# Performance work log

Hardware: AMD Instinct MI355X
Metric: run time of the kernel (lower is better)

Reference implementation:

```python
import jax, jax.numpy as jnp
import numpy as np
from jax import lax

KS = 3            # kernel_size
K = 32            # cluster_num
NB = 32           # num_base_kernels
HID = 64          # mlp_hidden_dim
COUT = 64         # out_channels
MAX_ITER = 20
TOL = 0.005


def _unfold3(x):
    # torch nn.Unfold(k=3, pad=1): output channel order is (c, kh, kw)
    b, c, h, w = x.shape
    xp = jnp.pad(x, ((0, 0), (0, 0), (1, 1), (1, 1)))
    cols = [xp[:, :, i:i + h, j:j + w] for i in range(KS) for j in range(KS)]
    p = jnp.stack(cols, axis=2)  # [B, C, 9, H, W]
    return p.reshape(b, c * KS * KS, h * w).transpose(0, 2, 1)  # [B, HW, C*9]


def _kmeans_single(key, sample):
    # sample: [N, D]. Lloyd iterations with early stop on total center shift.
    n, d = sample.shape
    centers0 = sample[jax.random.permutation(key, n)[:K]]

    def assign(centers):
        d2 = (jnp.sum(sample * sample, 1, keepdims=True)
              - 2.0 * (sample @ centers.T)
              + jnp.sum(centers * centers, 1))
        return jnp.argmin(d2, axis=1)

    def body(carry):
        i, centers, _ = carry
        a = assign(centers)
        oh = jax.nn.one_hot(a, K, dtype=sample.dtype)  # [N, K]
        counts = oh.sum(0)                             # [K]
        sums = oh.T @ sample                           # [K, D]
        new = jnp.where(counts[:, None] > 0,
                        sums / jnp.maximum(counts, 1.0)[:, None],
                        centers)
        shift = jnp.sum(jnp.linalg.norm(new - centers, axis=1))
        return (i + 1, new, shift)

    def cond(carry):
        i, _, shift = carry
        return jnp.logical_and(i < MAX_ITER, shift >= TOL * n)

    init = (jnp.int32(0), centers0, jnp.asarray(jnp.inf, sample.dtype))
    _, centers, _ = lax.while_loop(cond, body, init)
    return assign(centers)


def _kmeans(features):
    keys = jax.random.split(jax.random.key(42), features.shape[0])
    return jax.vmap(_kmeans_single)(keys, features)


def _mlp(x, w1, b1, w2, b2, w3, b3):
    h = jax.nn.relu(x @ w1 + b1)
    h = jax.nn.relu(h @ w2 + b2)
    return h @ w3 + b3


def setup_inputs() -> dict:
    key = jax.random.key(0)
    ks = jax.random.split(key, 16)
    B, C, H, W = 2, 32, 64, 64
    F = C * KS * KS
    fan = 1.0 / np.sqrt(F)
    fanh = 1.0 / np.sqrt(HID)
    return {
        'x': jax.random.normal(ks[0], (B, C, H, W), jnp.float32),
        'base_kernels': jax.random.normal(ks[1], (NB, F, COUT), jnp.float32) * np.sqrt(2.0 / F),
        'kg_w1': jax.random.normal(ks[2], (F, HID), jnp.float32) * fan,
        'kg_b1': jnp.zeros((HID,), jnp.float32),
        'kg_w2': jax.random.normal(ks[3], (HID, HID), jnp.float32) * fanh,
        'kg_b2': jnp.zeros((HID,), jnp.float32),
        'kg_w3': jax.random.normal(ks[4], (HID, NB), jnp.float32) * fanh,
        'kg_b3': jnp.zeros((NB,), jnp.float32),
        'bg_w1': jax.random.normal(ks[5], (F, HID), jnp.float32) * fan,
        'bg_b1': jnp.zeros((HID,), jnp.float32),
        'bg_w2': jax.random.normal(ks[6], (HID, HID), jnp.float32) * fanh,
        'bg_b2': jnp.zeros((HID,), jnp.float32),
        'bg_w3': jax.random.normal(ks[7], (HID, COUT), jnp.float32) * fanh,
        'bg_b3': jnp.zeros((COUT,), jnp.float32),
    }


def reference(x, base_kernels, kg_w1, kg_b1, kg_w2, kg_b2, kg_w3, kg_b3,
              bg_w1, bg_b1, bg_w2, bg_b2, bg_w3, bg_b3):
    B, C, H, W = x.shape
    patches = _unfold3(x)  # [B, P, F] with F = C*9
    P = patches.shape[1]
    # observation features: mean over kernel area per channel
    obs = patches.reshape(B, P, C, KS * KS).mean(-1)  # [B, P, C]
    idx = _kmeans(obs)  # [B, P] int cluster assignments

    # per-cluster centers of the full patch features (scatter-mean)
    oh = jax.nn.one_hot(idx, K, dtype=patches.dtype)          # [B, P, K]
    sums = jnp.einsum('bpk,bpf->bkf', oh, patches)            # [B, K, F]
    counts = jnp.maximum(oh.sum(1), 1.0)                      # [B, K]
    centers = sums / counts[:, :, None]                       # [B, K, F]

    # adaptive kernels = softmax-mixture of base kernels
    attn = jax.nn.softmax(_mlp(centers, kg_w1, kg_b1, kg_w2, kg_b2, kg_w3, kg_b3), axis=-1)  # [B,K,NB]
    kernels = jnp.einsum('bkn,nfc->bkfc', attn, base_kernels)  # [B, K, F, COUT]
    biases = _mlp(centers, bg_w1, bg_b1, bg_w2, bg_b2, bg_w3, bg_b3)  # [B, K, COUT]

    # combine: out[b,p] = patches[b,p] @ kernels[b, idx[b,p]] + biases[b, idx[b,p]]
    bidx = jnp.arange(B)[:, None]
    wtok = kernels[bidx, idx]   # [B, P, F, COUT]
    btok = biases[bidx, idx]    # [B, P, COUT]
    out = jnp.einsum('bpf,bpfc->bpc', patches, wtok) + btok
    out = out.transpose(0, 2, 1).reshape(B, COUT, H, W)
    return (out, idx)
```

## Files before the change

kernel.cpp:

```cpp
#include <hip/hip_runtime.h>
#include <hip/hip_bf16.h>
#include <vector>
#include <algorithm>
#include <utility>
#include <stdint.h>

#define BB 2
#define PP 4096
#define FF 288
#define KK 32
#define NBASE 32
#define HID 64
#define COUT 64
#define NWG_KM 32
#define SUBS 16
#define OUT_ELEMS 524288

#define THREEFRY_PARTITIONABLE 1

typedef unsigned short u16;

#define OFF_IDX    512
#define OFF_ATTN   33280
#define OFF_BIAS   41472
#define OFF_PART   57856
#define OFF_CNTS   320000
#define OFF_CPART  328192
#define OFF_WG     1544704
#define OFF_BAR2   3904000

struct InitIdx { int v[2][32]; };

__device__ __forceinline__ float bf2f(u16 u){
  union { unsigned int i; float f; } cv; cv.i = ((unsigned int)u) << 16; return cv.f;
}
__device__ __forceinline__ u16 f2bf(float f){
  union { float f; unsigned int i; } cv; cv.f = f;
  unsigned int x = cv.i;
  unsigned int r = (x + 0x7FFFu + ((x >> 16) & 1u)) >> 16;
  return (u16)r;
}
__device__ __forceinline__ float u_lo(unsigned int u){
  union { unsigned int i; float f; } cv; cv.i = u << 16; return cv.f;
}
__device__ __forceinline__ float u_hi(unsigned int u){
  union { unsigned int i; float f; } cv; cv.i = u & 0xFFFF0000u; return cv.f;
}

__device__ __forceinline__ void st_agent(float* p, float v){
  __hip_atomic_store(reinterpret_cast<unsigned int*>(p), __float_as_uint(v),
                     __ATOMIC_RELAXED, __HIP_MEMORY_SCOPE_AGENT);
}
__device__ __forceinline__ float ld_agent(const float* p){
  unsigned int u = __hip_atomic_load(reinterpret_cast<const unsigned int*>(p),
                                     __ATOMIC_RELAXED, __HIP_MEMORY_SCOPE_AGENT);
  return __uint_as_float(u);
}

template<bool BF>
__device__ __forceinline__ float ld(const void* p, size_t i){
  if constexpr (BF) { return bf2f(((const u16*)p)[i]); }
  else              { return ((const float*)p)[i]; }
}
template<bool BF>
__device__ __forceinline__ void st(void* p, size_t i, float v){
  if constexpr (BF) { ((u16*)p)[i] = f2bf(v); }
  else              { ((float*)p)[i] = v; }
}

template<bool BF>
__device__ __forceinline__ float obs_chan(const void* x, size_t bi, int h, int w){
  float s = 0.f;
  #pragma unroll
  for (int dh=-1; dh<=1; ++dh){
    int hh = h + dh;
    #pragma unroll
    for (int dw=-1; dw<=1; ++dw){
      int ww = w + dw;
      float v = 0.f;
      if ((unsigned)hh < 64u && (unsigned)ww < 64u) v = ld<BF>(x, bi + (hh<<6) + ww);
      s += v;
    }
  }
  return s / 9.0f;
}

__device__ __forceinline__ void gbar16(int* slots, int mb, int sub, int epoch){
  asm volatile("s_waitcnt vmcnt(0)" ::: "memory");
  __syncthreads();
  const int t = threadIdx.x;
  if (t == 0)
    __hip_atomic_store(&slots[(mb*16 + sub)*16], epoch, __ATOMIC_RELAXED, __HIP_MEMORY_SCOPE_AGENT);
  if (t < 16){
    while (__hip_atomic_load(&slots[(mb*16 + t)*16], __ATOMIC_RELAXED, __HIP_MEMORY_SCOPE_AGENT) < epoch){}
  }
  __atomic_signal_fence(__ATOMIC_SEQ_CST);
  __syncthreads();
}

__global__ __launch_bounds__(256) void kDetect(const void* __restrict__ x, int* flag,
                                               int* slots){
  __shared__ int cnt;
  if (threadIdx.x == 0) cnt = 0;
  for (int i = threadIdx.x; i < 512; i += 256) slots[i] = 0;
  __syncthreads();
  const u16* p = (const u16*)x;
  int bad = 0;
  for (int i = threadIdx.x; i < 1024; i += 256){
    u16 u = p[2*i];
    unsigned e = (u >> 7) & 0xFFu;
    if (e >= 131u) ++bad;
  }
  atomicAdd(&cnt, bad);
  __syncthreads();
  if (threadIdx.x == 0) *flag = (cnt < 102) ? 1 : 0;
}

template<bool BF>
__device__ void kB_body(const void* __restrict__ x,
                        float* __restrict__ part,
                        float* __restrict__ cnts,
                        int* __restrict__ idxg,
                        void* __restrict__ dout,
                        int* __restrict__ slots,
                        const InitIdx& ii,
                        float* obs_st,
                        float* cent,
                        float* cc_s,
                        int*   a_loc,
                        float* sq,
                        float* snorm,
                        float* cntsh,
                        float* acc8,
                        float* cnt8){
  const int t   = threadIdx.x;
  const int wg  = blockIdx.x;
  const int mb  = wg >> 4;
  const int sub = wg & 15;
  const int pg  = sub*256 + t;
  const int d   = t & 31, oct = t >> 5;

  float o[32];
  {
    int h = pg >> 6, w = pg & 63;
    size_t xb = (size_t)mb << 17;
    for (int c=0; c<32; ++c){
      float v = obs_chan<BF>(x, xb + ((size_t)c<<12), h, w);
      o[c] = v; obs_st[t*33 + c] = v;
    }
  }
  if (t < 32){
    int q = ii.v[mb][t];
    int qh = q >> 6, qw = q & 63;
    size_t xq = (size_t)mb << 17;
    for (int c=0; c<32; ++c) cent[t*32 + c] = obs_chan<BF>(x, xq + ((size_t)c<<12), qh, qw);
  }
  __syncthreads();

  float ss = 0.f;
  #pragma unroll
  for (int dd=0; dd<32; ++dd) ss = fmaf(o[dd], o[dd], ss);

  bool act = true;
  int parity = 0;

  for (int it=0; it<20 && act; ++it){
    if (t < 32){
      float s = 0.f;
      #pragma unroll
      for (int dd=0; dd<32; ++dd){ float v = cent[t*32 + dd]; s = fmaf(v,v,s); }
      cc_s[t] = s;
    }
    __syncthreads();
    float best = 3.0e38f; int bk = 0;
    for (int k=0; k<32; k+=4){
      const float4* c0 = (const float4*)&cent[(k  )*32];
      const float4* c1 = (const float4*)&cent[(k+1)*32];
      const float4* c2 = (const float4*)&cent[(k+2)*32];
      const float4* c3 = (const float4*)&cent[(k+3)*32];
      float dt0=0.f, dt1=0.f, dt2=0.f, dt3=0.f;
      #pragma unroll
      for (int q=0; q<8; ++q){
        float4 a0 = c0[q], a1 = c1[q], a2 = c2[q], a3 = c3[q];
        float o0 = o[q*4+0], o1 = o[q*4+1], o2 = o[q*4+2], o3 = o[q*4+3];
        dt0 = fmaf(o0,a0.x,dt0); dt0 = fmaf(o1,a0.y,dt0); dt0 = fmaf(o2,a0.z,dt0); dt0 = fmaf(o3,a0.w,dt0);
        dt1 = fmaf(o0,a1.x,dt1); dt1 = fmaf(o1,a1.y,dt1); dt1 = fmaf(o2,a1.z,dt1); dt1 = fmaf(o3,a1.w,dt1);
        dt2 = fmaf(o0,a2.x,dt2); dt2 = fmaf(o1,a2.y,dt2); dt2 = fmaf(o2,a2.z,dt2); dt2 = fmaf(o3,a2.w,dt2);
        dt3 = fmaf(o0,a3.x,dt3); dt3 = fmaf(o1,a3.y,dt3); dt3 = fmaf(o2,a3.z,dt3); dt3 = fmaf(o3,a3.w,dt3);
      }
      float di0 = (ss - 2.0f*dt0) + cc_s[k];
      float di1 = (ss - 2.0f*dt1) + cc_s[k+1];
      float di2 = (ss - 2.0f*dt2) + cc_s[k+2];
      float di3 = (ss - 2.0f*dt3) + cc_s[k+3];
      if (di0 < best){ best = di0; bk = k; }
      if (di1 < best){ best = di1; bk = k+1; }
      if (di2 < best){ best = di2; bk = k+2; }
      if (di3 < best){ best = di3; bk = k+3; }
    }
    a_loc[t] = bk;
    __syncthreads();
    for (int e=t; e<8*32*33; e+=256) acc8[e] = 0.f;
    cnt8[t] = 0.f;
    __syncthreads();
    {
      const int p0 = oct*32;
      int kcur = a_loc[p0];
      float racc = 0.f; int rl = 0;
      for (int i=0; i<32; ++i){
        int kp = a_loc[p0+i];
        float v = obs_st[(p0+i)*33 + d];
        if (kp != kcur){
          acc8[(oct*32 + kcur)*33 + d] += racc;
          if (d == 0) cnt8[oct*32 + kcur] += (float)rl;
          racc = 0.f; rl = 0; kcur = kp;
        }
        racc += v; ++rl;
      }
      acc8[(oct*32 + kcur)*33 + d] += racc;
      if (d == 0) cnt8[oct*32 + kcur] += (float)rl;
    }
    __syncthreads();
    float* Pg = part + ((size_t)((parity*2 + mb)*SUBS + sub))*1024;
    {
      float r0=0.f, r1=0.f, r2=0.f, r3=0.f;
      #pragma unroll
      for (int o2=0; o2<8; ++o2){
        r0 += acc8[(o2*32 + oct      )*33 + d];
        r1 += acc8[(o2*32 + oct + 8  )*33 + d];
        r2 += acc8[(o2*32 + oct + 16 )*33 + d];
        r3 += acc8[(o2*32 + oct + 24 )*33 + d];
      }
      st_agent(&Pg[(oct     )*32 + d], r0);
      st_agent(&Pg[(oct + 8 )*32 + d], r1);
      st_agent(&Pg[(oct + 16)*32 + d], r2);
      st_agent(&Pg[(oct + 24)*32 + d], r3);
    }
    if (t < 32){
      float c = 0.f;
      #pragma unroll
      for (int o2=0; o2<8; ++o2) c += cnt8[o2*32 + t];
      st_agent(&cnts[((size_t)((parity*2 + mb)*SUBS + sub))*32 + t], c);
    }
    gbar16(slots, mb, sub, it+1);
    {
      const float* Pb = part + (size_t)((parity*2 + mb)*SUBS)*1024;
      const float* Cb = cnts + (size_t)((parity*2 + mb)*SUBS)*32;
      if (t < 32){
        float s = 0.f;
        #pragma unroll
        for (int si=0; si<SUBS; ++si) s += ld_agent(&Cb[si*32 + t]);
        cntsh[t] = s;
      }
      __syncthreads();
      {
        int k = t >> 3, d4 = (t & 7) * 4;
        float vx = 0.f, vy = 0.f, vz = 0.f, vw = 0.f;
        #pragma unroll
        for (int si=0; si<SUBS; ++si){
          const float* pp = &Pb[si*1024 + k*32 + d4];
          float a0 = ld_agent(pp+0);
          float a1 = ld_agent(pp+1);
          float a2 = ld_agent(pp+2);
          float a3 = ld_agent(pp+3);
          vx += a0; vy += a1; vz += a2; vw += a3;
        }
        float cn = cntsh[k];
        float den = fmaxf(cn, 1.f);
        bool pos = cn > 0.f;
        float o0 = cent[k*32 + d4+0], o1 = cent[k*32 + d4+1];
        float o2 = cent[k*32 + d4+2], o3 = cent[k*32 + d4+3];
        float n0 = pos ? (vx / den) : o0;
        float n1 = pos ? (vy / den) : o1;
        float n2 = pos ? (vz / den) : o2;
        float n3 = pos ? (vw / den) : o3;
        float e0 = n0-o0, e1 = n1-o1, e2 = n2-o2, e3 = n3-o3;
        sq[k*32 + d4+0] = e0*e0; sq[k*32 + d4+1] = e1*e1;
        sq[k*32 + d4+2] = e2*e2; sq[k*32 + d4+3] = e3*e3;
        cent[k*32 + d4+0] = n0; cent[k*32 + d4+1] = n1;
        cent[k*32 + d4+2] = n2; cent[k*32 + d4+3] = n3;
      }
      __syncthreads();
      if (t < 32){
        float s = 0.f;
        #pragma unroll
        for (int dd=0; dd<32; ++dd) s += sq[t*32 + dd];
        snorm[t] = sqrtf(s);
      }
      __syncthreads();
      float sh = 0.f;
      for (int k=0;k<32;++k) sh += snorm[k];
      act = ((it+1) < 20) && ((double)sh >= 20.48);
      __syncthreads();
    }
    parity ^= 1;
  }
  if (t == 0)
    __hip_atomic_store(&slots[(mb*16 + sub)*16], 0x7FFFFFFF, __ATOMIC_RELAXED, __HIP_MEMORY_SCOPE_AGENT);
  __syncthreads();
  if (t < 32){
    float s = 0.f;
    #pragma unroll
    for (int dd=0; dd<32; ++dd){ float v = cent[t*32 + dd]; s = fmaf(v,v,s); }
    cc_s[t] = s;
  }
  __syncthreads();
  float best = 3.0e38f; int bk = 0;
  for (int k=0; k<32; k+=4){
    const float4* c0 = (const float4*)&cent[(k  )*32];
    const float4* c1 = (const float4*)&cent[(k+1)*32];
    const float4* c2 = (const float4*)&cent[(k+2)*32];
    const float4* c3 = (const float4*)&cent[(k+3)*32];
    float dt0=0.f, dt1=0.f, dt2=0.f, dt3=0.f;
    #pragma unroll
    for (int q=0; q<8; ++q){
      float4 a0 = c0[q], a1 = c1[q], a2 = c2[q], a3 = c3[q];
      float o0 = o[q*4+0], o1 = o[q*4+1], o2 = o[q*4+2], o3 = o[q*4+3];
      dt0 = fmaf(o0,a0.x,dt0); dt0 = fmaf(o1,a0.y,dt0); dt0 = fmaf(o2,a0.z,dt0); dt0 = fmaf(o3,a0.w,dt0);
      dt1 = fmaf(o0,a1.x,dt1); dt1 = fmaf(o1,a1.y,dt1); dt1 = fmaf(o2,a1.z,dt1); dt1 = fmaf(o3,a1.w,dt1);
      dt2 = fmaf(o0,a2.x,dt2); dt2 = fmaf(o1,a2.y,dt2); dt2 = fmaf(o2,a2.z,dt2); dt2 = fmaf(o3,a2.w,dt2);
      dt3 = fmaf(o0,a3.x,dt3); dt3 = fmaf(o1,a3.y,dt3); dt3 = fmaf(o2,a3.z,dt3); dt3 = fmaf(o3,a3.w,dt3);
    }
    float di0 = (ss - 2.0f*dt0) + cc_s[k];
    float di1 = (ss - 2.0f*dt1) + cc_s[k+1];
    float di2 = (ss - 2.0f*dt2) + cc_s[k+2];
    float di3 = (ss - 2.0f*dt3) + cc_s[k+3];
    if (di0 < best){ best = di0; bk = k; }
    if (di1 < best){ best = di1; bk = k+1; }
    if (di2 < best){ best = di2; bk = k+2; }
    if (di3 < best){ best = di3; bk = k+3; }
  }
  idxg[mb*PP + pg] = bk;
  st<BF>(dout, (size_t)OUT_ELEMS + mb*PP + pg, (float)bk);
}

__global__ __launch_bounds__(256) void kB(const void* x, float* part, float* cnts,
                                          int* idxg, void* dout,
                                          int* slots,
                                          const int* flag, InitIdx ii){
  __shared__ __align__(16) float obs_st[256*33];
  __shared__ __align__(16) float cent[32*32];
  __shared__ float cc_s[32];
  __shared__ int   a_loc[256];
  __shared__ float sq[32*32];
  __shared__ float snorm[32];
  __shared__ float cntsh[32];
  __shared__ float acc8[8*32*33];
  __shared__ float cnt8[8*32];
  if (*flag) kB_body<true >(x, part, cnts, idxg, dout, slots, ii,
                            obs_st, cent, cc_s, a_loc, sq, snorm, cntsh, acc8, cnt8);
  else       kB_body<false>(x, part, cnts, idxg, dout, slots, ii,
                            obs_st, cent, cc_s, a_loc, sq, snorm, cntsh, acc8, cnt8);
}

template<bool BF>
__device__ void kC_body(const void* __restrict__ x,
                        const int* __restrict__ idxg,
                        float* __restrict__ cpartJ,
                        float* __restrict__ acc,
                        int* __restrict__ idxsh){
  int wgid = blockIdx.x;
  int cg = wgid / 9, j = wgid % 9;
  int b = cg >> 4, pc = cg & 15;
  int t = threadIdx.x;
  for (int e=t; e<32*33; e+=256) acc[e] = 0.f;
  idxsh[t] = idxg[b*PP + pc*256 + t];
  __syncthreads();

  int dh = j/3 - 1, dw = j%3 - 1;
  int gp = (pc << 8) + t;
  int h = gp >> 6, w = gp & 63;
  int k = idxsh[t];
  int hh = h + dh, ww = w + dw;
  bool ok = ((unsigned)hh < 64u) && ((unsigned)ww < 64u);
  size_t boff = ((size_t)b << 17) + (hh << 6) + ww;

  #pragma unroll 4
  for (int c=0; c<32; ++c){
    float v = ok ? ld<BF>(x, boff + ((size_t)c << 12)) : 0.f;
    atomicAdd(&acc[k*33 + c], v);
  }
  if (j == 0) atomicAdd(&acc[k*33 + 32], 1.0f);
  __syncthreads();
  float* cp = cpartJ + (size_t)wgid*(32*33);
  for (int e=t; e<32*33; e+=256) cp[e] = acc[e];
}

__global__ __launch_bounds__(256) void kC(const void* x, const int* idxg,
                                          float* cpartJ, const int* flag){
  __shared__ float acc[32*33];
  __shared__ int   idxsh[256];
  if (*flag) kC_body<true >(x, idxg, cpartJ, acc, idxsh);
  else       kC_body<false>(x, idxg, cpartJ, acc, idxsh);
}

template<bool BF>
__device__ void kD_body(const float* __restrict__ cpartJ,
                        const void* kg_w1, const void* kg_b1,
                        const void* kg_w2, const void* kg_b2,
                        const void* kg_w3, const void* kg_b3,
                        const void* bg_w1, const void* bg_b1,
                        const void* bg_w2, const void* bg_b2,
                        const void* bg_w3, const void* bg_b3,
                        float* __restrict__ attn,
                        float* __restrict__ biasO,
                        float* __restrict__ row,
                        float* __restrict__ h1,
                        float* __restrict__ h2,
                        float* __restrict__ lgs){
  int wg = blockIdx.x; int b = wg >> 5; int k = wg & 31;
  int t = threadIdx.x;
  float cnt = 0.f;
  for (int ch=0; ch<16; ++ch)
    cnt += cpartJ[(size_t)((b*16+ch)*9)*(32*33) + k*33 + 32];
  float den = fmaxf(cnt, 1.f);
  for (int f=t; f<FF; f+=64){
    int c = f / 9, j = f % 9;
    float s = 0.f;
    for (int ch=0; ch<16; ++ch)
      s += cpartJ[(size_t)((b*16+ch)*9 + j)*(32*33) + k*33 + c];
    row[f] = s / den;
  }
  __syncthreads();

  {
    float s = 0.f;
    #pragma unroll 8
    for (int f=0; f<FF; ++f) s = fmaf(row[f], ld<BF>(kg_w1, f*HID + t), s);
    h1[t] = fmaxf(s + ld<BF>(kg_b1, t), 0.f);
  }
  __syncthreads();
  {
    float s = 0.f;
    #pragma unroll 8
    for (int h=0; h<HID; ++h) s = fmaf(h1[h], ld<BF>(kg_w2, h*HID + t), s);
    h2[t] = fmaxf(s + ld<BF>(kg_b2, t), 0.f);
  }
  __syncthreads();
  if (t < 32){
    float s = 0.f;
    #pragma unroll 8
    for (int h=0; h<HID; ++h) s = fmaf(h2[h], ld<BF>(kg_w3, h*NBASE + t), s);
    lgs[t] = s + ld<BF>(kg_b3, t);
  }
  __syncthreads();
  if (t < 32){
    float mx = -3.0e38f;
    for (int i=0;i<NBASE;++i) mx = fmaxf(mx, lgs[i]);
    float se = 0.f;
    for (int i=0;i<NBASE;++i) se += expf(lgs[i]-mx);
    attn[wg*NBASE + t] = expf(lgs[t]-mx) / se;
  }
  __syncthreads();
  {
    float s = 0.f;
    #pragma unroll 8
    for (int f=0; f<FF; ++f) s = fmaf(row[f], ld<BF>(bg_w1, f*HID + t), s);
    h1[t] = fmaxf(s + ld<BF>(bg_b1, t), 0.f);
  }
  __syncthreads();
  {
    float s = 0.f;
    #pragma unroll 8
    for (int h=0; h<HID; ++h) s = fmaf(h1[h], ld<BF>(bg_w2, h*HID + t), s);
    h2[t] = fmaxf(s + ld<BF>(bg_b2, t), 0.f);
  }
  __syncthreads();
  {
    float s = 0.f;
    #pragma unroll 8
    for (int h=0; h<HID; ++h) s = fmaf(h2[h], ld<BF>(bg_w3, h*COUT + t), s);
    biasO[wg*COUT + t] = s + ld<BF>(bg_b3, t);
  }
}

__global__ __launch_bounds__(64) void kD(const float* cpartJ,
                                         const void* kg_w1, const void* kg_b1,
                                         const void* kg_w2, const void* kg_b2,
                                         const void* kg_w3, const void* kg_b3,
                                         const void* bg_w1, const void* bg_b1,
                                         const void* bg_w2, const void* bg_b2,
                                         const void* bg_w3, const void* bg_b3,
                                         float* attn, float* biasO, const int* flag){
  __shared__ float row[FF];
  __shared__ float h1[64];
  __shared__ float h2[64];
  __shared__ float lgs[32];
  if (*flag) kD_body<true >(cpartJ, kg_w1,kg_b1,kg_w2,kg_b2,kg_w3,kg_b3,
                            bg_w1,bg_b1,bg_w2,bg_b2,bg_w3,bg_b3, attn, biasO, row,h1,h2,lgs);
  else       kD_body<false>(cpartJ, kg_w1,kg_b1,kg_w2,kg_b2,kg_w3,kg_b3,
                            bg_w1,bg_b1,bg_w2,bg_b2,bg_w3,bg_b3, attn, biasO, row,h1,h2,lgs);
}

template<bool BF>
__device__ void kE_body(const void* __restrict__ base,
                        const float* __restrict__ attn,
                        u16* __restrict__ Wg,
                        float* __restrict__ at,
                        float* __restrict__ tile){
  int wg = blockIdx.x;
  int fq = wg & 3, bk = wg >> 2;
  int t = threadIdx.x;
  if (t < 32) at[t] = attn[bk*NBASE + t];
  __syncthreads();
  int f0 = fq*72;
  for (int e=t; e<72*64; e+=256){
    int fl = e >> 6, c = e & 63;
    size_t bi = (size_t)(f0 + fl)*COUT + c;
    float s = 0.f;
    #pragma unroll 8
    for (int n=0; n<NBASE; ++n)
      s = fmaf(at[n], ld<BF>(base, bi + (size_t)n*FF*COUT), s);
    tile[fl*65 + c] = s;
  }
  __syncthreads();
  for (int e=t; e<72*64; e+=256){
    int c = e / 72, fl = e % 72;
    Wg[(size_t)bk*(64*FF) + (size_t)c*FF + f0 + fl] = f2bf(tile[fl*65 + c]);
  }
}

__global__ __launch_bounds__(256) void kE(const void* base, const float* attn,
                                          u16* Wg, const int* flag){
  __shared__ float at[32];
  __shared__ float tile[72*65];
  if (*flag) kE_body<true >(base, attn, Wg, at, tile);
  else       kE_body<false>(base, attn, Wg, at, tile);
}

template<bool BF>
__device__ void kF_body(const void* __restrict__ x,
                        const int* __restrict__ idxg,
                        const u16* __restrict__ Wg,
                        const float* __restrict__ biasO,
                        void* __restrict__ dout,
                        u16* __restrict__ patch,
                        float* __restrict__ outT){
  int wg = blockIdx.x;
  int q = wg & 3, h = (wg >> 2) & 63, b = wg >> 8;
  int t = threadIdx.x, wv = t >> 6, lane = t & 63;
  int w0 = q << 4;

  for (int e=t; e<16*FF; e+=256){
    int pl = e & 15, fe = e >> 4;
    int c = fe / 9, j = fe % 9;
    int hh = h + j/3 - 1, ww = w0 + pl + (j%3) - 1;
    float v = 0.f;
    if ((unsigned)hh < 64u && (unsigned)ww < 64u)
      v = ld<BF>(x, ((size_t)b << 17) + ((size_t)c << 12) + (hh<<6) + ww);
    patch[pl*296 + fe] = f2bf(v);
  }
  __syncthreads();

  #pragma unroll
  for (int i=0; i<4; ++i){
    int pl = (wv << 2) + i;
    int p = (h << 6) + w0 + pl;
    int k = idxg[(b << 12) + p];
    const uint4* Wp = (const uint4*)(Wg + ((size_t)((b << 5) + k)*64 + lane)*FF);
    const uint4* Pp = (const uint4*)(patch + pl*296);
    float acc = 0.f;
    #pragma unroll 6
    for (int j=0; j<36; ++j){
      uint4 wv4 = Wp[j];
      uint4 pv4 = Pp[j];
      acc = fmaf(u_lo(pv4.x), u_lo(wv4.x), acc);
      acc = fmaf(u_hi(pv4.x), u_hi(wv4.x), acc);
      acc = fmaf(u_lo(pv4.y), u_lo(wv4.y), acc);
      acc = fmaf(u_hi(pv4.y), u_hi(wv4.y), acc);
      acc = fmaf(u_lo(pv4.z), u_lo(wv4.z), acc);
      acc = fmaf(u_hi(pv4.z), u_hi(wv4.z), acc);
      acc = fmaf(u_lo(pv4.w), u_lo(wv4.w), acc);
      acc = fmaf(u_hi(pv4.w), u_hi(wv4.w), acc);
    }
    float bias = biasO[((b << 5) + k)*COUT + lane];
    outT[lane*17 + pl] = acc + bias;
  }
  __syncthreads();

  for (int e=t; e<1024; e+=256){
    int cout = e >> 4, pl = e & 15;
    st<BF>(dout, (((size_t)(b << 6) + cout) << 12) + (h << 6) + w0 + pl,
           outT[cout*17 + pl]);
  }
}

__global__ __launch_bounds__(256) void kF(const void* x, const int* idxg,
                                          const u16* Wg, const float* biasO,
                                          void* dout, const int* flag){
  __shared__ u16   patch[16*296];
  __shared__ float outT[64*17];
  if (*flag) kF_body<true >(x, idxg, Wg, biasO, dout, patch, outT);
  else       kF_body<false>(x, idxg, Wg, biasO, dout, patch, outT);
}

static inline uint32_t rotl32(uint32_t x, int d){ return (x<<d)|(x>>(32-d)); }
static void tf_block(uint32_t k0,uint32_t k1,uint32_t x0,uint32_t x1,uint32_t&o0,uint32_t&o1){
  uint32_t ks2 = k0 ^ k1 ^ 0x1BD11BDAu;
  uint32_t v0 = x0 + k0, v1 = x1 + k1;
  const int ra[4]={13,15,26,6}, rb[4]={17,29,16,24};
  #define R4(r) for(int i_=0;i_<4;++i_){ v0 += v1; v1 = rotl32(v1,(r)[i_]); v1 ^= v0; }
  R4(ra); v0 += k1;  v1 += ks2 + 1u;
  R4(rb); v0 += ks2; v1 += k0  + 2u;
  R4(ra); v0 += k0;  v1 += k1  + 3u;
  R4(rb); v0 += k1;  v1 += ks2 + 4u;
  R4(ra); v0 += ks2; v1 += k0  + 5u;
  #undef R4
  o0 = v0; o1 = v1;
}
struct KP{ uint32_t a, b; };
static void tf_split(KP k, KP& first, KP& second){
#if THREEFRY_PARTITIONABLE
  uint32_t a0,b0,a1,b1;
  tf_block(k.a,k.b, 0u,0u, a0,b0);
  tf_block(k.a,k.b, 0u,1u, a1,b1);
  first  = KP{a0,b0};
  second = KP{a1,b1};
#else
  uint32_t a0,b0,a1,b1;
  tf_block(k.a,k.b, 0u,2u, a0,b0);
  tf_block(k.a,k.b, 1u,3u, a1,b1);
  first  = KP{a0,a1};
  second = KP{b0,b1};
#endif
}
static void random_bits_4096(KP k, std::vector<uint32_t>& bits){
// ... 15 lines not shown
  std::vector<uint32_t> bits(4096);
  std::vector<std::pair<uint32_t,int>> pr(4096);
  KP k = key;
  for (int r=0;r<2;++r){
    KP nk, sk; tf_split(k, nk, sk); k = nk;
    random_bits_4096(sk, bits);
    for (int i=0;i<4096;++i) pr[i] = std::make_pair(bits[i], vals[i]);
    std::stable_sort(pr.begin(), pr.end(),
        [](const std::pair<uint32_t,int>& a, const std::pair<uint32_t,int>& c){ return a.first < c.first; });
    for (int i=0;i<4096;++i) vals[i] = pr[i].second;
  }
  for (int j=0;j<32;++j) out32[j] = vals[j];
}

extern "C" void kernel_launch(void* const* d_in, const int* in_sizes, int n_in,
                              void* d_out, int out_size, void* d_ws, size_t ws_size,
                              hipStream_t stream) {
  const void* x     = d_in[0];
  const void* base  = d_in[1];
  const void* kg_w1 = d_in[2];
  const void* kg_b1 = d_in[3];
  const void* kg_w2 = d_in[4];
  const void* kg_b2 = d_in[5];
  const void* kg_w3 = d_in[6];
  const void* kg_b3 = d_in[7];
  const void* bg_w1 = d_in[8];
  const void* bg_b1 = d_in[9];
  const void* bg_w2 = d_in[10];
  const void* bg_b2 = d_in[11];
  const void* bg_w3 = d_in[12];
  const void* bg_b3 = d_in[13];

  char* ws = (char*)d_ws;
  int*   flag  = (int*)(ws + 64);
  int*   idxg  = (int*)(ws + OFF_IDX);
  float* attn  = (float*)(ws + OFF_ATTN);
  float* biasO = (float*)(ws + OFF_BIAS);
  float* part  = (float*)(ws + OFF_PART);
  float* cnts  = (float*)(ws + OFF_CNTS);
  float* cpartJ= (float*)(ws + OFF_CPART);
  u16*   Wg    = (u16*)(ws + OFF_WG);
  int*   slots = (int*)(ws + OFF_BAR2);

  InitIdx ii;
  KP root = KP{0u, 42u};
  KP kb0, kb1; tf_split(root, kb0, kb1);
  perm_first32(kb0, ii.v[0]);
  perm_first32(kb1, ii.v[1]);

  kDetect<<<1, 256, 0, stream>>>(x, flag, slots);
  kB<<<NWG_KM, 256, 0, stream>>>(x, part, cnts, idxg, d_out, slots, flag, ii);
  kC<<<288, 256, 0, stream>>>(x, idxg, cpartJ, flag);
  kD<<<64, 64, 0, stream>>>(cpartJ,
                            kg_w1, kg_b1, kg_w2, kg_b2, kg_w3, kg_b3,
                            bg_w1, bg_b1, bg_w2, bg_b2, bg_w3, bg_b3,
                            attn, biasO, flag);
  kE<<<256, 256, 0, stream>>>(base, attn, Wg, flag);
  kF<<<512, 256, 0, stream>>>(x, idxg, Wg, biasO, d_out, flag);
}
```

Before: 288.4 us.

## Split k-means kernel into 128 single-wave workgroups with two-level reduction barrier

The k-means kernel now launches 128 workgroups of 64 threads instead of 32 of 256, so each workgroup owns a quarter of its previous points. Per-iteration centroid sums are combined in two stages. Three helper workgroups publish raw partials to a leader, which folds them into one slot per 256-point segment. All 16 segment leaders then signal a second barrier that every workgroup waits on before recomputing centers. The aim is to spread the latency-bound Lloyd iterations over more compute units and shrink the per-workgroup shared-memory reduction, at the cost of an extra synchronization stage and more global partial traffic per iteration.

```diff
diff --git a/kernel.cpp b/kernel.cpp
--- a/kernel.cpp
+++ b/kernel.cpp
@@ -12,8 +12,7 @@
 #define NBASE 32
 #define HID 64
 #define COUT 64
-#define NWG_KM 32
-#define SUBS 16
+#define NWG_KM 128
 #define OUT_ELEMS 524288
 
 #define THREEFRY_PARTITIONABLE 1
@@ -23,8 +22,7 @@
 #define OFF_IDX    512
 #define OFF_ATTN   33280
 #define OFF_BIAS   41472
-#define OFF_PART   57856
-#define OFF_CNTS   320000
+#define OFF_SI     57856
 #define OFF_CPART  328192
 #define OFF_WG     1544704
 #define OFF_BAR2   3904000
@@ -55,6 +53,19 @@
   unsigned int u = __hip_atomic_load(reinterpret_cast<const unsigned int*>(p),
                                      __ATOMIC_RELAXED, __HIP_MEMORY_SCOPE_AGENT);
   return __uint_as_float(u);
+}
+__device__ __forceinline__ void ld_agent2(const float* p, float& a, float& b){
+  unsigned long long u = __hip_atomic_load(
+      reinterpret_cast<const unsigned long long*>(p),
+      __ATOMIC_RELAXED, __HIP_MEMORY_SCOPE_AGENT);
+  a = __uint_as_float((unsigned int)(u & 0xFFFFFFFFull));
+  b = __uint_as_float((unsigned int)(u >> 32));
+}
+__device__ __forceinline__ void st_slot(int* p, int v){
+  __hip_atomic_store(p, v, __ATOMIC_RELAXED, __HIP_MEMORY_SCOPE_AGENT);
+}
+__device__ __forceinline__ int ld_slot(const int* p){
+  return __hip_atomic_load(p, __ATOMIC_RELAXED, __HIP_MEMORY_SCOPE_AGENT);
 }
 
 template<bool BF>
@@ -85,24 +96,11 @@
   return s / 9.0f;
 }
 
-__device__ __forceinline__ void gbar16(int* slots, int mb, int sub, int epoch){
-  asm volatile("s_waitcnt vmcnt(0)" ::: "memory");
-  __syncthreads();
-  const int t = threadIdx.x;
-  if (t == 0)
-    __hip_atomic_store(&slots[(mb*16 + sub)*16], epoch, __ATOMIC_RELAXED, __HIP_MEMORY_SCOPE_AGENT);
-  if (t < 16){
-    while (__hip_atomic_load(&slots[(mb*16 + t)*16], __ATOMIC_RELAXED, __HIP_MEMORY_SCOPE_AGENT) < epoch){}
-  }
-  __atomic_signal_fence(__ATOMIC_SEQ_CST);
-  __syncthreads();
-}
-
 __global__ __launch_bounds__(256) void kDetect(const void* __restrict__ x, int* flag,
                                                int* slots){
   __shared__ int cnt;
   if (threadIdx.x == 0) cnt = 0;
-  for (int i = threadIdx.x; i < 512; i += 256) slots[i] = 0;
+  for (int i = threadIdx.x; i < 2560; i += 256) slots[i] = 0;
   __syncthreads();
   const u16* p = (const u16*)x;
   int bad = 0;
@@ -118,11 +116,12 @@
 
 template<bool BF>
 __device__ void kB_body(const void* __restrict__ x,
-                        float* __restrict__ part,
-                        float* __restrict__ cnts,
+                        float* __restrict__ sI,
+                        float* __restrict__ raw,
                         int* __restrict__ idxg,
                         void* __restrict__ dout,
-                        int* __restrict__ slots,
+                        int* __restrict__ slotsA,
+                        int* __restrict__ slotsB,
                         const InitIdx& ii,
                         float* obs_st,
                         float* cent,
@@ -131,21 +130,22 @@
                         float* sq,
                         float* snorm,
                         float* cntsh,
-                        float* acc8,
-                        float* cnt8){
-  const int t   = threadIdx.x;
-  const int wg  = blockIdx.x;
-  const int mb  = wg >> 4;
-  const int sub = wg & 15;
-  const int pg  = sub*256 + t;
-  const int d   = t & 31, oct = t >> 5;
+                        float* acc2){
+  const int t    = threadIdx.x;
+  const int wgid = blockIdx.x;
+  const int mb   = wgid >> 6;
+  const int w    = wgid & 63;
+  const int si   = w >> 2;
+  const int qt   = w & 3;
+  const int pg   = si*256 + qt*64 + t;
+  const int d    = t & 31, l = t >> 5;
 
   float o[32];
   {
-    int h = pg >> 6, w = pg & 63;
+    int h = pg >> 6, wp = pg & 63;
     size_t xb = (size_t)mb << 17;
     for (int c=0; c<32; ++c){
-      float v = obs_chan<BF>(x, xb + ((size_t)c<<12), h, w);
+      float v = obs_chan<BF>(x, xb + ((size_t)c<<12), h, wp);
       o[c] = v; obs_st[t*33 + c] = v;
     }
   }
@@ -199,104 +199,106 @@
     }
     a_loc[t] = bk;
     __syncthreads();
-    for (int e=t; e<8*32*33; e+=256) acc8[e] = 0.f;
-    cnt8[t] = 0.f;
+    for (int e=t; e<2112; e+=64) acc2[e] = 0.f;
     __syncthreads();
     {
-      const int p0 = oct*32;
+      const int p0 = l*32;
       int kcur = a_loc[p0];
       float racc = 0.f; int rl = 0;
       for (int i=0; i<32; ++i){
         int kp = a_loc[p0+i];
         float v = obs_st[(p0+i)*33 + d];
         if (kp != kcur){
-          acc8[(oct*32 + kcur)*33 + d] += racc;
-          if (d == 0) cnt8[oct*32 + kcur] += (float)rl;
+          acc2[(l*32 + kcur)*33 + d] += racc;
+          if (d == 0) acc2[(l*32 + kcur)*33 + 32] += (float)rl;
           racc = 0.f; rl = 0; kcur = kp;
         }
         racc += v; ++rl;
       }
-      acc8[(oct*32 + kcur)*33 + d] += racc;
-      if (d == 0) cnt8[oct*32 + kcur] += (float)rl;
+      acc2[(l*32 + kcur)*33 + d] += racc;
+      if (d == 0) acc2[(l*32 + kcur)*33 + 32] += (float)rl;
     }
     __syncthreads();
-    float* Pg = part + ((size_t)((parity*2 + mb)*SUBS + sub))*1024;
+
+    if (qt != 0){
+      float* rb = raw + ((size_t)((mb*16 + si)*6 + (2*qt - 2)))*1056;
+      for (int e=t; e<2112; e+=64) st_agent(&rb[e], acc2[e]);
+      asm volatile("s_waitcnt vmcnt(0)" ::: "memory");
+      __syncthreads();
+      if (t == 0) st_slot(&slotsA[wgid*16], it+1);
+    } else {
+      if (t < 3){
+        while (ld_slot(&slotsA[(wgid+1+t)*16]) < it+1){}
+      }
+      __atomic_signal_fence(__ATOMIC_SEQ_CST);
+      __syncthreads();
+      const float* rb = raw + ((size_t)((mb*16 + si)*6))*1056;
+      float* sip = sI + ((size_t)(((parity*2 + mb)*16) + si))*1056;
+      for (int e=t; e<1056; e+=64){
+        float s = acc2[e] + acc2[1056 + e];
+        #pragma unroll
+        for (int j=0; j<6; ++j) s += ld_agent(&rb[j*1056 + e]);
+        int k = e / 33, c = e - k*33;
+        if (c < 32) st_agent(&sip[k*32 + c], s);
+        else        st_agent(&sip[1024 + k], s);
+      }
+      asm volatile("s_waitcnt vmcnt(0)" ::: "memory");
+      __syncthreads();
+      if (t == 0) st_slot(&slotsB[(mb*16 + si)*16], it+1);
+    }
+    if (t < 16){
+      while (ld_slot(&slotsB[(mb*16 + t)*16]) < it+1){}
+    }
+    __atomic_signal_fence(__ATOMIC_SEQ_CST);
+    __syncthreads();
     {
-      float r0=0.f, r1=0.f, r2=0.f, r3=0.f;
+      const float* Sb = sI + ((size_t)((parity*2 + mb)*16))*1056;
+      int k = t >> 1, d0 = (t & 1)*16;
+      float v0=0.f,v1=0.f,v2=0.f,v3=0.f,v4=0.f,v5=0.f,v6=0.f,v7=0.f;
+      float v8=0.f,v9=0.f,va=0.f,vb=0.f,vc=0.f,vd=0.f,ve=0.f,vf=0.f;
+      float cn = 0.f;
+      for (int s2=0; s2<16; ++s2){
+        const float* p = &Sb[s2*1056 + k*32 + d0];
+        float x0,x1;
+        ld_agent2(p+ 0,x0,x1); v0+=x0; v1+=x1;
+        ld_agent2(p+ 2,x0,x1); v2+=x0; v3+=x1;
+        ld_agent2(p+ 4,x0,x1); v4+=x0; v5+=x1;
+        ld_agent2(p+ 6,x0,x1); v6+=x0; v7+=x1;
+        ld_agent2(p+ 8,x0,x1); v8+=x0; v9+=x1;
+        ld_agent2(p+10,x0,x1); va+=x0; vb+=x1;
+        ld_agent2(p+12,x0,x1); vc+=x0; vd+=x1;
+        ld_agent2(p+14,x0,x1); ve+=x0; vf+=x1;
+        if ((t & 1) == 0) cn += ld_agent(&Sb[s2*1056 + 1024 + k]);
+      }
+      if ((t & 1) == 0) cntsh[k] = cn;
+      __syncthreads();
+      float cnt = cntsh[k];
+      float den = fmaxf(cnt, 1.f);
+      bool pos = cnt > 0.f;
+      float vv[16] = {v0,v1,v2,v3,v4,v5,v6,v7,v8,v9,va,vb,vc,vd,ve,vf};
       #pragma unroll
-      for (int o2=0; o2<8; ++o2){
-        r0 += acc8[(o2*32 + oct      )*33 + d];
-        r1 += acc8[(o2*32 + oct + 8  )*33 + d];
-        r2 += acc8[(o2*32 + oct + 16 )*33 + d];
-        r3 += acc8[(o2*32 + oct + 24 )*33 + d];
+      for (int j=0; j<16; ++j){
+        float oo = cent[k*32 + d0 + j];
+        float n  = pos ? (vv[j]/den) : oo;
+        float e  = n - oo;
+        sq[k*32 + d0 + j]   = e*e;
+        cent[k*32 + d0 + j] = n;
       }
-      st_agent(&Pg[(oct     )*32 + d], r0);
-      st_agent(&Pg[(oct + 8 )*32 + d], r1);
-      st_agent(&Pg[(oct + 16)*32 + d], r2);
-      st_agent(&Pg[(oct + 24)*32 + d], r3);
-    }
+    }
+    __syncthreads();
     if (t < 32){
-      float c = 0.f;
+      float s = 0.f;
       #pragma unroll
-      for (int o2=0; o2<8; ++o2) c += cnt8[o2*32 + t];
-      st_agent(&cnts[((size_t)((parity*2 + mb)*SUBS + sub))*32 + t], c);
-    }
-    gbar16(slots, mb, sub, it+1);
-    {
-      const float* Pb = part + (size_t)((parity*2 + mb)*SUBS)*1024;
-      const float* Cb = cnts + (size_t)((parity*2 + mb)*SUBS)*32;
-      if (t < 32){
-        float s = 0.f;
-        #pragma unroll
-        for (int si=0; si<SUBS; ++si) s += ld_agent(&Cb[si*32 + t]);
-        cntsh[t] = s;
-      }
-      __syncthreads();
-      {
-        int k = t >> 3, d4 = (t & 7) * 4;
-        float vx = 0.f, vy = 0.f, vz = 0.f, vw = 0.f;
-        #pragma unroll
-        for (int si=0; si<SUBS; ++si){
-          const float* pp = &Pb[si*1024 + k*32 + d4];
-          float a0 = ld_agent(pp+0);
-          float a1 = ld_agent(pp+1);
-          float a2 = ld_agent(pp+2);
-          float a3 = ld_agent(pp+3);
-          vx += a0; vy += a1; vz += a2; vw += a3;
-        }
-        float cn = cntsh[k];
-        float den = fmaxf(cn, 1.f);
-        bool pos = cn > 0.f;
-        float o0 = cent[k*32 + d4+0], o1 = cent[k*32 + d4+1];
-        float o2 = cent[k*32 + d4+2], o3 = cent[k*32 + d4+3];
-        float n0 = pos ? (vx / den) : o0;
-        float n1 = pos ? (vy / den) : o1;
-        float n2 = pos ? (vz / den) : o2;
-        float n3 = pos ? (vw / den) : o3;
-        float e0 = n0-o0, e1 = n1-o1, e2 = n2-o2, e3 = n3-o3;
-        sq[k*32 + d4+0] = e0*e0; sq[k*32 + d4+1] = e1*e1;
-        sq[k*32 + d4+2] = e2*e2; sq[k*32 + d4+3] = e3*e3;
-        cent[k*32 + d4+0] = n0; cent[k*32 + d4+1] = n1;
-        cent[k*32 + d4+2] = n2; cent[k*32 + d4+3] = n3;
-      }
-      __syncthreads();
-      if (t < 32){
-        float s = 0.f;
-        #pragma unroll
-        for (int dd=0; dd<32; ++dd) s += sq[t*32 + dd];
-        snorm[t] = sqrtf(s);
-      }
-      __syncthreads();
-      float sh = 0.f;
-      for (int k=0;k<32;++k) sh += snorm[k];
-      act = ((it+1) < 20) && ((double)sh >= 20.48);
-      __syncthreads();
-    }
+      for (int dd=0; dd<32; ++dd) s += sq[t*32 + dd];
+      snorm[t] = sqrtf(s);
+    }
+    __syncthreads();
+    float sh = 0.f;
+    for (int k=0;k<32;++k) sh += snorm[k];
+    act = ((it+1) < 20) && ((double)sh >= 20.48);
+    __syncthreads();
     parity ^= 1;
   }
-  if (t == 0)
-    __hip_atomic_store(&slots[(mb*16 + sub)*16], 0x7FFFFFFF, __ATOMIC_RELAXED, __HIP_MEMORY_SCOPE_AGENT);
-  __syncthreads();
   if (t < 32){
     float s = 0.f;
     #pragma unroll
@@ -333,23 +335,22 @@
   st<BF>(dout, (size_t)OUT_ELEMS + mb*PP + pg, (float)bk);
 }
 
-__global__ __launch_bounds__(256) void kB(const void* x, float* part, float* cnts,
-                                          int* idxg, void* dout,
-                                          int* slots,
-                                          const int* flag, InitIdx ii){
-  __shared__ __align__(16) float obs_st[256*33];
+__global__ __launch_bounds__(64) void kB(const void* x, float* sI, float* raw,
+                                         int* idxg, void* dout,
+                                         int* slotsA, int* slotsB,
+                                         const int* flag, InitIdx ii){
+  __shared__ __align__(16) float obs_st[64*33];
   __shared__ __align__(16) float cent[32*32];
   __shared__ float cc_s[32];
-  __shared__ int   a_loc[256];
+  __shared__ int   a_loc[64];
   __shared__ float sq[32*32];
   __shared__ float snorm[32];
   __shared__ float cntsh[32];
-  __shared__ float acc8[8*32*33];
-  __shared__ float cnt8[8*32];
-  if (*flag) kB_body<true >(x, part, cnts, idxg, dout, slots, ii,
-                            obs_st, cent, cc_s, a_loc, sq, snorm, cntsh, acc8, cnt8);
-  else       kB_body<false>(x, part, cnts, idxg, dout, slots, ii,
-                            obs_st, cent, cc_s, a_loc, sq, snorm, cntsh, acc8, cnt8);
+  __shared__ __align__(16) float acc2[2*1056];
+  if (*flag) kB_body<true >(x, sI, raw, idxg, dout, slotsA, slotsB, ii,
+                            obs_st, cent, cc_s, a_loc, sq, snorm, cntsh, acc2);
+  else       kB_body<false>(x, sI, raw, idxg, dout, slotsA, slotsB, ii,
+                            obs_st, cent, cc_s, a_loc, sq, snorm, cntsh, acc2);
 }
 
 template<bool BF>
@@ -676,11 +677,12 @@
   int*   idxg  = (int*)(ws + OFF_IDX);
   float* attn  = (float*)(ws + OFF_ATTN);
   float* biasO = (float*)(ws + OFF_BIAS);
-  float* part  = (float*)(ws + OFF_PART);
-  float* cnts  = (float*)(ws + OFF_CNTS);
+  float* sI    = (float*)(ws + OFF_SI);
   float* cpartJ= (float*)(ws + OFF_CPART);
+  float* raw   = (float*)(ws + OFF_CPART);
   u16*   Wg    = (u16*)(ws + OFF_WG);
-  int*   slots = (int*)(ws + OFF_BAR2);
+  int*   slotsA= (int*)(ws + OFF_BAR2);
+  int*   slotsB= (int*)(ws + OFF_BAR2 + 8192);
 
   InitIdx ii;
   KP root = KP{0u, 42u};
@@ -688,8 +690,8 @@
   perm_first32(kb0, ii.v[0]);
   perm_first32(kb1, ii.v[1]);
 
-  kDetect<<<1, 256, 0, stream>>>(x, flag, slots);
-  kB<<<NWG_KM, 256, 0, stream>>>(x, part, cnts, idxg, d_out, slots, flag, ii);
+  kDetect<<<1, 256, 0, stream>>>(x, flag, slotsA);
+  kB<<<NWG_KM, 64, 0, stream>>>(x, sI, raw, idxg, d_out, slotsA, slotsB, flag, ii);
   kC<<<288, 256, 0, stream>>>(x, idxg, cpartJ, flag);
   kD<<<64, 64, 0, stream>>>(cpartJ,
                             kg_w1, kg_b1, kg_w2, kg_b2, kg_w3, kg_b3,
```

Result: slower. 317.1 us (+10.0%).

## Fuse all stages into one persistent kernel with software grid barriers

Applied to the files above, without the earlier changes.

Replaces six separate launches (detect, kmeans, scatter-mean, MLP, kernel mixing, output conv) with a single 256-workgroup persistent kernel. Stages are separated by a spin-wait grid barrier on global slots. Dtype detection now runs redundantly in every block, and the barrier slots are cleared with a memset. The aim is to remove launch gaps and tail effects between small kernels. In exchange, it depends on all 256 blocks being co-resident and adds barrier latency, and the stages with few blocks leave most workgroups idle.

```diff
diff --git a/kernel.cpp b/kernel.cpp
--- a/kernel.cpp
+++ b/kernel.cpp
@@ -28,6 +28,7 @@
 #define OFF_CPART  328192
 #define OFF_WG     1544704
 #define OFF_BAR2   3904000
+#define OFF_GBAR   3906048
 
 struct InitIdx { int v[2][32]; };
 
@@ -55,6 +56,12 @@
   unsigned int u = __hip_atomic_load(reinterpret_cast<const unsigned int*>(p),
                                      __ATOMIC_RELAXED, __HIP_MEMORY_SCOPE_AGENT);
   return __uint_as_float(u);
+}
+__device__ __forceinline__ void st_slot(int* p, int v){
+  __hip_atomic_store(p, v, __ATOMIC_RELAXED, __HIP_MEMORY_SCOPE_AGENT);
+}
+__device__ __forceinline__ int ld_slot(const int* p){
+  return __hip_atomic_load(p, __ATOMIC_RELAXED, __HIP_MEMORY_SCOPE_AGENT);
 }
 
 template<bool BF>
@@ -89,35 +96,31 @@
   asm volatile("s_waitcnt vmcnt(0)" ::: "memory");
   __syncthreads();
   const int t = threadIdx.x;
-  if (t == 0)
-    __hip_atomic_store(&slots[(mb*16 + sub)*16], epoch, __ATOMIC_RELAXED, __HIP_MEMORY_SCOPE_AGENT);
+  if (t == 0) st_slot(&slots[(mb*16 + sub)*16], epoch);
   if (t < 16){
-    while (__hip_atomic_load(&slots[(mb*16 + t)*16], __ATOMIC_RELAXED, __HIP_MEMORY_SCOPE_AGENT) < epoch){}
+    while (ld_slot(&slots[(mb*16 + t)*16]) < epoch){}
   }
   __atomic_signal_fence(__ATOMIC_SEQ_CST);
   __syncthreads();
 }
 
-__global__ __launch_bounds__(256) void kDetect(const void* __restrict__ x, int* flag,
-                                               int* slots){
-  __shared__ int cnt;
-  if (threadIdx.x == 0) cnt = 0;
-  for (int i = threadIdx.x; i < 512; i += 256) slots[i] = 0;
-  __syncthreads();
-  const u16* p = (const u16*)x;
-  int bad = 0;
-  for (int i = threadIdx.x; i < 1024; i += 256){
-    u16 u = p[2*i];
-    unsigned e = (u >> 7) & 0xFFu;
-    if (e >= 131u) ++bad;
-  }
-  atomicAdd(&cnt, bad);
-  __syncthreads();
-  if (threadIdx.x == 0) *flag = (cnt < 102) ? 1 : 0;
-}
-
-template<bool BF>
-__device__ void kB_body(const void* __restrict__ x,
+__device__ __forceinline__ void gridbar(int* gslots, int wg, int phase){
+  __syncthreads();
+  __threadfence();
+  const int t = threadIdx.x;
+  if (t == 0) st_slot(&gslots[wg*4], phase);
+  if (t < 16){
+    for (int j = t*16; j < t*16 + 16; ++j){
+      while (ld_slot(&gslots[j*4]) < phase) __builtin_amdgcn_s_sleep(2);
+    }
+  }
+  __atomic_signal_fence(__ATOMIC_SEQ_CST);
+  __syncthreads();
+  __threadfence();
+}
+
+template<bool BF>
+__device__ void kB_body(int wg, const void* __restrict__ x,
                         float* __restrict__ part,
                         float* __restrict__ cnts,
                         int* __restrict__ idxg,
@@ -134,7 +137,6 @@
                         float* acc8,
                         float* cnt8){
   const int t   = threadIdx.x;
-  const int wg  = blockIdx.x;
   const int mb  = wg >> 4;
   const int sub = wg & 15;
   const int pg  = sub*256 + t;
@@ -294,8 +296,7 @@
     }
     parity ^= 1;
   }
-  if (t == 0)
-    __hip_atomic_store(&slots[(mb*16 + sub)*16], 0x7FFFFFFF, __ATOMIC_RELAXED, __HIP_MEMORY_SCOPE_AGENT);
+  if (t == 0) st_slot(&slots[(mb*16 + sub)*16], 0x7FFFFFFF);
   __syncthreads();
   if (t < 32){
     float s = 0.f;
@@ -333,32 +334,12 @@
   st<BF>(dout, (size_t)OUT_ELEMS + mb*PP + pg, (float)bk);
 }
 
-__global__ __launch_bounds__(256) void kB(const void* x, float* part, float* cnts,
-                                          int* idxg, void* dout,
-                                          int* slots,
-                                          const int* flag, InitIdx ii){
-  __shared__ __align__(16) float obs_st[256*33];
-  __shared__ __align__(16) float cent[32*32];
-  __shared__ float cc_s[32];
-  __shared__ int   a_loc[256];
-  __shared__ float sq[32*32];
-  __shared__ float snorm[32];
-  __shared__ float cntsh[32];
-  __shared__ float acc8[8*32*33];
-  __shared__ float cnt8[8*32];
-  if (*flag) kB_body<true >(x, part, cnts, idxg, dout, slots, ii,
-                            obs_st, cent, cc_s, a_loc, sq, snorm, cntsh, acc8, cnt8);
-  else       kB_body<false>(x, part, cnts, idxg, dout, slots, ii,
-                            obs_st, cent, cc_s, a_loc, sq, snorm, cntsh, acc8, cnt8);
-}
-
-template<bool BF>
-__device__ void kC_body(const void* __restrict__ x,
+template<bool BF>
+__device__ void kC_body(int wgid, const void* __restrict__ x,
                         const int* __restrict__ idxg,
                         float* __restrict__ cpartJ,
                         float* __restrict__ acc,
                         int* __restrict__ idxsh){
-  int wgid = blockIdx.x;
   int cg = wgid / 9, j = wgid % 9;
   int b = cg >> 4, pc = cg & 15;
   int t = threadIdx.x;
@@ -385,16 +366,8 @@
   for (int e=t; e<32*33; e+=256) cp[e] = acc[e];
 }
 
-__global__ __launch_bounds__(256) void kC(const void* x, const int* idxg,
-                                          float* cpartJ, const int* flag){
-  __shared__ float acc[32*33];
-  __shared__ int   idxsh[256];
-  if (*flag) kC_body<true >(x, idxg, cpartJ, acc, idxsh);
-  else       kC_body<false>(x, idxg, cpartJ, acc, idxsh);
-}
-
-template<bool BF>
-__device__ void kD_body(const float* __restrict__ cpartJ,
+template<bool BF>
+__device__ void kD_body(int wg, const float* __restrict__ cpartJ,
                         const void* kg_w1, const void* kg_b1,
                         const void* kg_w2, const void* kg_b2,
                         const void* kg_w3, const void* kg_b3,
@@ -407,29 +380,31 @@
                         float* __restrict__ h1,
                         float* __restrict__ h2,
                         float* __restrict__ lgs){
-  int wg = blockIdx.x; int b = wg >> 5; int k = wg & 31;
+  int b = wg >> 5; int k = wg & 31;
   int t = threadIdx.x;
-  float cnt = 0.f;
-  for (int ch=0; ch<16; ++ch)
-    cnt += cpartJ[(size_t)((b*16+ch)*9)*(32*33) + k*33 + 32];
-  float den = fmaxf(cnt, 1.f);
-  for (int f=t; f<FF; f+=64){
-    int c = f / 9, j = f % 9;
-    float s = 0.f;
+  if (t < 64){
+    float cnt = 0.f;
     for (int ch=0; ch<16; ++ch)
-      s += cpartJ[(size_t)((b*16+ch)*9 + j)*(32*33) + k*33 + c];
-    row[f] = s / den;
-  }
-  __syncthreads();
-
-  {
+      cnt += cpartJ[(size_t)((b*16+ch)*9)*(32*33) + k*33 + 32];
+    float den = fmaxf(cnt, 1.f);
+    for (int f=t; f<FF; f+=64){
+      int c = f / 9, j = f % 9;
+      float s = 0.f;
+      for (int ch=0; ch<16; ++ch)
+        s += cpartJ[(size_t)((b*16+ch)*9 + j)*(32*33) + k*33 + c];
+      row[f] = s / den;
+    }
+  }
+  __syncthreads();
+
+  if (t < 64){
     float s = 0.f;
     #pragma unroll 8
     for (int f=0; f<FF; ++f) s = fmaf(row[f], ld<BF>(kg_w1, f*HID + t), s);
     h1[t] = fmaxf(s + ld<BF>(kg_b1, t), 0.f);
   }
   __syncthreads();
-  {
+  if (t < 64){
     float s = 0.f;
     #pragma unroll 8
     for (int h=0; h<HID; ++h) s = fmaf(h1[h], ld<BF>(kg_w2, h*HID + t), s);
@@ -451,21 +426,21 @@
     attn[wg*NBASE + t] = expf(lgs[t]-mx) / se;
   }
   __syncthreads();
-  {
+  if (t < 64){
     float s = 0.f;
     #pragma unroll 8
     for (int f=0; f<FF; ++f) s = fmaf(row[f], ld<BF>(bg_w1, f*HID + t), s);
     h1[t] = fmaxf(s + ld<BF>(bg_b1, t), 0.f);
   }
   __syncthreads();
-  {
+  if (t < 64){
     float s = 0.f;
     #pragma unroll 8
     for (int h=0; h<HID; ++h) s = fmaf(h1[h], ld<BF>(bg_w2, h*HID + t), s);
     h2[t] = fmaxf(s + ld<BF>(bg_b2, t), 0.f);
   }
   __syncthreads();
-  {
+  if (t < 64){
     float s = 0.f;
     #pragma unroll 8
     for (int h=0; h<HID; ++h) s = fmaf(h2[h], ld<BF>(bg_w3, h*COUT + t), s);
@@ -473,31 +448,12 @@
   }
 }
 
-__global__ __launch_bounds__(64) void kD(const float* cpartJ,
-                                         const void* kg_w1, const void* kg_b1,
-                                         const void* kg_w2, const void* kg_b2,
-                                         const void* kg_w3, const void* kg_b3,
-                                         const void* bg_w1, const void* bg_b1,
-                                         const void* bg_w2, const void* bg_b2,
-                                         const void* bg_w3, const void* bg_b3,
-                                         float* attn, float* biasO, const int* flag){
-  __shared__ float row[FF];
-  __shared__ float h1[64];
-  __shared__ float h2[64];
-  __shared__ float lgs[32];
-  if (*flag) kD_body<true >(cpartJ, kg_w1,kg_b1,kg_w2,kg_b2,kg_w3,kg_b3,
-                            bg_w1,bg_b1,bg_w2,bg_b2,bg_w3,bg_b3, attn, biasO, row,h1,h2,lgs);
-  else       kD_body<false>(cpartJ, kg_w1,kg_b1,kg_w2,kg_b2,kg_w3,kg_b3,
-                            bg_w1,bg_b1,bg_w2,bg_b2,bg_w3,bg_b3, attn, biasO, row,h1,h2,lgs);
-}
-
-template<bool BF>
-__device__ void kE_body(const void* __restrict__ base,
+template<bool BF>
+__device__ void kE_body(int wg, const void* __restrict__ base,
                         const float* __restrict__ attn,
                         u16* __restrict__ Wg,
                         float* __restrict__ at,
                         float* __restrict__ tile){
-  int wg = blockIdx.x;
   int fq = wg & 3, bk = wg >> 2;
   int t = threadIdx.x;
   if (t < 32) at[t] = attn[bk*NBASE + t];
@@ -519,23 +475,14 @@
   }
 }
 
-__global__ __launch_bounds__(256) void kE(const void* base, const float* attn,
-                                          u16* Wg, const int* flag){
-  __shared__ float at[32];
-  __shared__ float tile[72*65];
-  if (*flag) kE_body<true >(base, attn, Wg, at, tile);
-  else       kE_body<false>(base, attn, Wg, at, tile);
-}
-
-template<bool BF>
-__device__ void kF_body(const void* __restrict__ x,
+template<bool BF>
+__device__ void kF_body(int wg, const void* __restrict__ x,
                         const int* __restrict__ idxg,
                         const u16* __restrict__ Wg,
                         const float* __restrict__ biasO,
                         void* __restrict__ dout,
                         u16* __restrict__ patch,
                         float* __restrict__ outT){
-  int wg = blockIdx.x;
   int q = wg & 3, h = (wg >> 2) & 63, b = wg >> 8;
   int t = threadIdx.x, wv = t >> 6, lane = t & 63;
   int w0 = q << 4;
@@ -582,15 +529,92 @@
     st<BF>(dout, (((size_t)(b << 6) + cout) << 12) + (h << 6) + w0 + pl,
            outT[cout*17 + pl]);
   }
-}
-
-__global__ __launch_bounds__(256) void kF(const void* x, const int* idxg,
-                                          const u16* Wg, const float* biasO,
-                                          void* dout, const int* flag){
-  __shared__ u16   patch[16*296];
-  __shared__ float outT[64*17];
-  if (*flag) kF_body<true >(x, idxg, Wg, biasO, dout, patch, outT);
-  else       kF_body<false>(x, idxg, Wg, biasO, dout, patch, outT);
+  __syncthreads();
+}
+
+template<bool BF>
+__device__ void mega_body(int wg, const void* x, const void* base,
+                          const void* kg_w1, const void* kg_b1,
+                          const void* kg_w2, const void* kg_b2,
+                          const void* kg_w3, const void* kg_b3,
+                          const void* bg_w1, const void* bg_b1,
+                          const void* bg_w2, const void* bg_b2,
+                          const void* bg_w3, const void* bg_b3,
+                          void* dout,
+                          int* idxg, float* attn, float* biasO,
+                          float* part, float* cnts, float* cpartJ, u16* Wg,
+                          int* slots, int* gslots,
+                          const InitIdx& ii, char* sm){
+  if (wg < NWG_KM){
+    kB_body<BF>(wg, x, part, cnts, idxg, dout, slots, ii,
+                (float*)(sm + 0), (float*)(sm + 67584), (float*)(sm + 76800),
+                (int*)(sm + 75776), (float*)(sm + 71680), (float*)(sm + 76928),
+                (float*)(sm + 77056), (float*)(sm + 33792), (float*)(sm + 77184));
+  }
+  gridbar(gslots, wg, 1);
+
+  kC_body<BF>(wg, x, idxg, cpartJ, (float*)(sm + 0), (int*)(sm + 4224));
+  if (wg >= 224){
+    __syncthreads();
+    kC_body<BF>(wg + 32, x, idxg, cpartJ, (float*)(sm + 0), (int*)(sm + 4224));
+  }
+  gridbar(gslots, wg, 2);
+
+  if (wg < 64){
+    kD_body<BF>(wg, cpartJ, kg_w1,kg_b1,kg_w2,kg_b2,kg_w3,kg_b3,
+                bg_w1,bg_b1,bg_w2,bg_b2,bg_w3,bg_b3, attn, biasO,
+                (float*)(sm + 0), (float*)(sm + 1152), (float*)(sm + 1408),
+                (float*)(sm + 1664));
+  }
+  gridbar(gslots, wg, 3);
+
+  kE_body<BF>(wg, base, attn, Wg, (float*)(sm + 0), (float*)(sm + 128));
+  gridbar(gslots, wg, 4);
+
+  kF_body<BF>(wg,       x, idxg, Wg, biasO, dout, (u16*)(sm + 0), (float*)(sm + 9472));
+  kF_body<BF>(wg + 256, x, idxg, Wg, biasO, dout, (u16*)(sm + 0), (float*)(sm + 9472));
+}
+
+__global__ __launch_bounds__(256) void kMega(const void* x, const void* base,
+                          const void* kg_w1, const void* kg_b1,
+                          const void* kg_w2, const void* kg_b2,
+                          const void* kg_w3, const void* kg_b3,
+                          const void* bg_w1, const void* bg_b1,
+                          const void* bg_w2, const void* bg_b2,
+                          const void* bg_w3, const void* bg_b3,
+                          void* dout,
+                          int* idxg, float* attn, float* biasO,
+                          float* part, float* cnts, float* cpartJ, u16* Wg,
+                          int* slots, int* gslots, InitIdx ii){
+  __shared__ __align__(16) char sm[78336];
+  __shared__ int cntS;
+  const int t = threadIdx.x;
+  const int wg = blockIdx.x;
+
+  if (t == 0) cntS = 0;
+  __syncthreads();
+  {
+    const u16* p = (const u16*)x;
+    int bad = 0;
+    for (int i = t; i < 1024; i += 256){
+      u16 u = p[2*i];
+      unsigned e = (u >> 7) & 0xFFu;
+      if (e >= 131u) ++bad;
+    }
+    atomicAdd(&cntS, bad);
+  }
+  __syncthreads();
+  const bool BF = (cntS < 102);
+  __syncthreads();
+
+  if (BF) mega_body<true >(wg, x, base, kg_w1,kg_b1,kg_w2,kg_b2,kg_w3,kg_b3,
+                           bg_w1,bg_b1,bg_w2,bg_b2,bg_w3,bg_b3, dout,
+                           idxg, attn, biasO, part, cnts, cpartJ, Wg,
+                           slots, gslots, ii, sm);
+  else    mega_body<false>(wg, x, base, kg_w1,kg_b1,kg_w2,kg_b2,kg_w3,kg_b3,
+                           bg_w1,bg_b1,bg_w2,bg_b2,bg_w3,bg_b3, dout,
+                           idxg, attn, biasO, part, cnts, cpartJ, Wg,
+                           slots, gslots, ii, sm);
 }
 
 static inline uint32_t rotl32(uint32_t x, int d){ return (x<<d)|(x>>(32-d)); }
@@ -672,7 +696,6 @@
   const void* bg_b3 = d_in[13];
 
   char* ws = (char*)d_ws;
-  int*   flag  = (int*)(ws + 64);
   int*   idxg  = (int*)(ws + OFF_IDX);
   float* attn  = (float*)(ws + OFF_ATTN);
   float* biasO = (float*)(ws + OFF_BIAS);
@@ -681,6 +704,7 @@
   float* cpartJ= (float*)(ws + OFF_CPART);
   u16*   Wg    = (u16*)(ws + OFF_WG);
   int*   slots = (int*)(ws + OFF_BAR2);
+  int*   gslots= (int*)(ws + OFF_GBAR);
 
   InitIdx ii;
   KP root = KP{0u, 42u};
@@ -688,13 +712,10 @@
   perm_first32(kb0, ii.v[0]);
   perm_first32(kb1, ii.v[1]);
 
-  kDetect<<<1, 256, 0, stream>>>(x, flag, slots);
-  kB<<<NWG_KM, 256, 0, stream>>>(x, part, cnts, idxg, d_out, slots, flag, ii);
-  kC<<<288, 256, 0, stream>>>(x, idxg, cpartJ, flag);
-  kD<<<64, 64, 0, stream>>>(cpartJ,
-                            kg_w1, kg_b1, kg_w2, kg_b2, kg_w3, kg_b3,
-                            bg_w1, bg_b1, bg_w2, bg_b2, bg_w3, bg_b3,
-                            attn, biasO, flag);
-  kE<<<256, 256, 0, stream>>>(base, attn, Wg, flag);
-  kF<<<512, 256, 0, stream>>>(x, idxg, Wg, biasO, d_out, flag);
-}
+  hipMemsetAsync(ws + OFF_BAR2, 0, 6144, stream);
+  kMega<<<256, 256, 0, stream>>>(x, base,
+                                 kg_w1, kg_b1, kg_w2, kg_b2, kg_w3, kg_b3,
+                                 bg_w1, bg_b1, bg_w2, bg_b2, bg_w3, bg_b3,
+                                 d_out, idxg, attn, biasO, part, cnts, cpartJ, Wg,
+                                 slots, gslots, ii);
+}
```

Result: slower. 412.6 us (+43.1%).
